# Performance work log

Hardware: AMD Instinct MI355X
Metric: run time of the kernel (lower is better)

## Reference

```python
import jax, jax.numpy as jnp
import numpy as np

IN_FEATURES = 4096
OUT_FEATURES = 4096
ALPHA = 0.008

def setup_inputs() -> dict:
    key = jax.random.key(0)
    k_x, k_w = jax.random.split(key)
    # int8-valued activations and weights, stored as their natural int/float forms
    x = jax.random.randint(k_x, (4, 2048, IN_FEATURES), -127, 128, dtype=jnp.int32)
    weight = jax.random.randint(k_w, (OUT_FEATURES, IN_FEATURES), -127, 128, dtype=jnp.int32).astype(jnp.float32)
    bias = jnp.zeros((1, OUT_FEATURES), dtype=jnp.float32)  # fp16 in module; fp32 here for math
    alpha = jnp.float32(ALPHA)
    return {"x": x, "weight": weight, "bias": bias, "alpha": alpha}

def reference(x, weight, bias, alpha):
    # x: [B, S, in], weight: [out, in] (int8 values cast to fp32), bias: [1, out]
    # In the original, rand_elements/mask_mul are zeros so hybrid path == plain path:
    #   y = F.linear(x.float(), weight.float()); fp_y = y*alpha + bias
    x_shape = x.shape
    xf = x.reshape(-1, x_shape[-1]).astype(jnp.float32)  # [N, in]
    y = jnp.einsum('ni,oi->no', xf, weight)              # fp32 GEMM, as in the module
    fp_y = y * alpha + bias
    out = jnp.clip(jnp.round(fp_y), -128, 127).astype(jnp.int8)
    return out.reshape(*x_shape[:-1], -1)
```

## Files before the change

kernel.cpp:

```cpp
#include <hip/hip_runtime.h>
#include <stdint.h>

typedef int int32x4  __attribute__((ext_vector_type(4)));
typedef int int32x16 __attribute__((ext_vector_type(16)));

#define IN_F   4096
#define OUT_F  4096
#define ROWS   8192

#define BM 256
#define BN 256
#define BK 64
#define NT (IN_F / BK)
#define ABUF 16384
#define LDS_TOTAL (4 * ABUF)

#define GLOAD_LDS16(g, l)                                                      \
  __builtin_amdgcn_global_load_lds(                                            \
      (const __attribute__((address_space(1))) void*)(g),                      \
      (__attribute__((address_space(3))) void*)(l), 16, 0, 0)

__device__ __forceinline__ int pack4i(int a, int b, int c, int d) {
  return (a & 0xff) | ((b & 0xff) << 8) | ((c & 0xff) << 16) | (d << 24);
}

#define CVT_BLOCKS 2048
#define CVT_NA 1048576
#define CVT_NTOT 1572864
__global__ void __launch_bounds__(256) cvt_kernel(const int4* __restrict__ x,
                                                  const float4* __restrict__ w,
                                                  int4* __restrict__ oa,
                                                  int4* __restrict__ ob) {
  for (size_t c = (size_t)blockIdx.x * 256 + threadIdx.x; c < CVT_NTOT;
       c += (size_t)CVT_BLOCKS * 256) {
    if (c < CVT_NA) {
      const int block = (int)(c >> 5), r = (int)(c & 31);
      const int m = (block >> 7) * 32 + r, kb = block & 127;
      const int4* src = x + (size_t)m * 1024 + kb * 8;
      int p[8];
#pragma unroll
      for (int j = 0; j < 8; ++j) {
        int4 a = src[j];
        p[j] = pack4i(a.x, a.y, a.z, a.w);
      }
      oa[(size_t)block * 64 + r]      = make_int4(p[0], p[1], p[2], p[3]);
      oa[(size_t)block * 64 + r + 32] = make_int4(p[4], p[5], p[6], p[7]);
    } else {
      const size_t c2 = c - CVT_NA;
      const int block = (int)(c2 >> 5), r = (int)(c2 & 31);
      const int n = (block >> 7) * 32 + r, kb = block & 127;
      const float4* src = w + (size_t)n * 1024 + kb * 8;
      int p[8];
#pragma unroll
      for (int j = 0; j < 8; ++j) {
        float4 a = src[j];
        p[j] = pack4i(__float2int_rn(a.x), __float2int_rn(a.y),
                      __float2int_rn(a.z), __float2int_rn(a.w));
      }
      ob[(size_t)block * 64 + r]      = make_int4(p[0], p[1], p[2], p[3]);
      ob[(size_t)block * 64 + r + 32] = make_int4(p[4], p[5], p[6], p[7]);
    }
  }
}

__global__ void __launch_bounds__(512) gemm_i8_kernel(
    const int8_t* __restrict__ A8p, const int8_t* __restrict__ B8p,
    const float* __restrict__ bias, const float* __restrict__ alpha_p,
    int* __restrict__ out) {
  extern __shared__ int8_t lds[];

  const int t    = threadIdx.x;
  const int wave = t >> 6;
  const int lane = t & 63;
  const int l31  = lane & 31;
  const int hi   = lane >> 5;
  const int wm   = wave >> 2;
  const int wn   = wave & 3;

  const int flat = blockIdx.y * gridDim.x + blockIdx.x;
  const int wid  = (flat & 7) * 64 + (flat >> 3);
  const int bn   = wid >> 5;
  const int bm   = wid & 31;

  const int mb0 = bm * 8 + (t >> 7);
  const int kbi = (t >> 6) & 1;
  const size_t aOff0 = ((size_t)mb0 * 128 + kbi) * 1024 + (size_t)(t & 63) * 16;
  const size_t aOff1 = ((size_t)(mb0 + 4) * 128 + kbi) * 1024 + (size_t)(t & 63) * 16;
  const int ldsT = t * 16;

  const int8_t* bPtr = B8p + (size_t)(bn * 8 + wn * 2) * 131072 + (size_t)lane * 16;

  const int aLds = wm * 8192 + lane * 16;

  int32x16 acc[4][2] = {};
  int32x4 af[4][2];
  int32x4 Bc00, Bc01, Bc10, Bc11, Bn00, Bn01, Bn10, Bn11;

#define ISSUE_A(TILE)                                                          \
  do {                                                                         \
    int8_t* _b = lds + ((TILE) & 3) * ABUF;                                    \
    GLOAD_LDS16(A8p + aOff0 + (size_t)(TILE) * 2048, _b + ldsT);               \
    GLOAD_LDS16(A8p + aOff1 + (size_t)(TILE) * 2048, _b + 8192 + ldsT);        \
  } while (0)

#define LOAD_B(TILE, B00, B01, B10, B11)                                       \
  do {                                                                         \
    const int8_t* _p = bPtr + (size_t)(TILE) * 2048;                           \
    B00 = *(const int32x4*)(_p);                                               \
    B01 = *(const int32x4*)(_p + 1024);                                        \
    B10 = *(const int32x4*)(_p + 131072);                                      \
    B11 = *(const int32x4*)(_p + 131072 + 1024);                               \
  } while (0)

#define READ_A(TILE)                                                           \
  do {                                                                         \
    const int8_t* _a = lds + ((TILE) & 3) * ABUF + aLds;                       \
    _Pragma("unroll") for (int mi = 0; mi < 4; ++mi) {                         \
      af[mi][0] = *(const int32x4*)(_a + mi * 2048);                           \
      af[mi][1] = *(const int32x4*)(_a + mi * 2048 + 1024);                    \
    }                                                                          \
  } while (0)

#define MFMA16(B00, B01, B10, B11)                                             \
  do {                                                                         \
    __builtin_amdgcn_s_setprio(1);                                             \
    _Pragma("unroll") for (int mi = 0; mi < 4; ++mi) {                         \
      acc[mi][0] = __builtin_amdgcn_mfma_i32_32x32x32_i8(af[mi][0], B00,       \
                                                         acc[mi][0], 0, 0, 0); \
      acc[mi][1] = __builtin_amdgcn_mfma_i32_32x32x32_i8(af[mi][0], B10,       \
                                                         acc[mi][1], 0, 0, 0); \
    }                                                                          \
    _Pragma("unroll") for (int mi = 0; mi < 4; ++mi) {                         \
      acc[mi][0] = __builtin_amdgcn_mfma_i32_32x32x32_i8(af[mi][1], B01,       \
                                                         acc[mi][0], 0, 0, 0); \
      acc[mi][1] = __builtin_amdgcn_mfma_i32_32x32x32_i8(af[mi][1], B11,       \
                                                         acc[mi][1], 0, 0, 0); \
    }                                                                          \
    __builtin_amdgcn_s_setprio(0);                                             \
  } while (0)

#define GATE2                                                                  \
  do {                                                                         \
    asm volatile("s_waitcnt vmcnt(2)" ::: "memory");                           \
    __builtin_amdgcn_s_barrier();                                              \
  } while (0)

  ISSUE_A(0);
  LOAD_B(0, Bc00, Bc01, Bc10, Bc11);
  ISSUE_A(1);
  GATE2;

  for (int tt = 0; tt < NT - 2; tt += 2) {
    LOAD_B(tt + 1, Bn00, Bn01, Bn10, Bn11);
    ISSUE_A(tt + 2);
    READ_A(tt);
    MFMA16(Bc00, Bc01, Bc10, Bc11);
    GATE2;

    LOAD_B(tt + 2, Bc00, Bc01, Bc10, Bc11);
    ISSUE_A(tt + 3);
    READ_A(tt + 1);
    MFMA16(Bn00, Bn01, Bn10, Bn11);
    GATE2;
  }
  LOAD_B(NT - 1, Bn00, Bn01, Bn10, Bn11);
  READ_A(NT - 2);
  MFMA16(Bc00, Bc01, Bc10, Bc11);
  asm volatile("s_waitcnt vmcnt(0)" ::: "memory");
  __builtin_amdgcn_s_barrier();
  READ_A(NT - 1);
  MFMA16(Bn00, Bn01, Bn10, Bn11);

  const float alpha = *alpha_p;
#pragma unroll
  for (int mi = 0; mi < 4; ++mi) {
    const int rowt = bm * BM + wm * 128 + mi * 32 + hi * 4;
#pragma unroll
    for (int ni = 0; ni < 2; ++ni) {
      const int col = bn * BN + wn * 64 + ni * 32 + l31;
      const float bv = bias[col];
#pragma unroll
      for (int r = 0; r < 16; ++r) {
        const int row = rowt + (r & 3) + 8 * (r >> 2);
        float v = rintf((float)acc[mi][ni][r] * alpha + bv);
        v = fminf(fmaxf(v, -128.f), 127.f);
        out[(size_t)row * OUT_F + col] = (int)v;
      }
    }
  }
#undef ISSUE_A
#undef LOAD_B
#undef READ_A
#undef MFMA16
#undef GATE2
}

extern "C" void kernel_launch(void* const* d_in, const int* in_sizes, int n_in,
                              void* d_out, int out_size, void* d_ws, size_t ws_size,
                              hipStream_t stream) {
  const int*   x     = (const int*)d_in[0];
  const float* w     = (const float*)d_in[1];
  const float* bias  = (const float*)d_in[2];
  const float* alpha = (const float*)d_in[3];
  int* out = (int*)d_out;

  int8_t* x8 = (int8_t*)d_ws;
  int8_t* w8 = x8 + (size_t)ROWS * IN_F;

  static bool attr_done = false;
  if (!attr_done) {
    (void)hipFuncSetAttribute(reinterpret_cast<const void*>(gemm_i8_kernel),
                              hipFuncAttributeMaxDynamicSharedMemorySize,
                              LDS_TOTAL);
    attr_done = true;
  }

  cvt_kernel<<<CVT_BLOCKS, 256, 0, stream>>>((const int4*)x, (const float4*)w,
                                             (int4*)x8, (int4*)w8);

  dim3 grid(OUT_F / BN, ROWS / BM);
  gemm_i8_kernel<<<grid, 512, LDS_TOTAL, stream>>>(x8, w8, bias, alpha, out);
}
```

Baseline: 417.0 us.

## Shrink GEMM tiles to 128x128 with 4 waves and remap convert kernel threads

The GEMM block tile goes from 256x256 with 8 waves to 128x128 with 4 waves, and each wave now holds a 64x64 output sub-tile. The LDS buffers shrink to match, and launch bounds ask for 3 blocks per CU. The aim is more blocks and better occupancy and load balance across CUs, at the cost of less data reuse per block and more global traffic for A and B. The convert kernel also changes its thread-to-element mapping so that each group of 8 adjacent threads handles 8 different k-blocks, which changes how its memory accesses coalesce.

```diff
diff --git a/kernel.cpp b/kernel.cpp
--- a/kernel.cpp
+++ b/kernel.cpp
@@ -8,11 +8,11 @@
 #define OUT_F  4096
 #define ROWS   8192
 
-#define BM 256
-#define BN 256
+#define BM 128
+#define BN 128
 #define BK 64
 #define NT (IN_F / BK)
-#define ABUF 16384
+#define ABUF 8192
 #define LDS_TOTAL (4 * ABUF)
 
 #define GLOAD_LDS16(g, l)                                                      \
@@ -31,10 +31,12 @@
                                                   const float4* __restrict__ w,
                                                   int4* __restrict__ oa,
                                                   int4* __restrict__ ob) {
-  for (size_t c = (size_t)blockIdx.x * 256 + threadIdx.x; c < CVT_NTOT;
-       c += (size_t)CVT_BLOCKS * 256) {
-    if (c < CVT_NA) {
-      const int block = (int)(c >> 5), r = (int)(c & 31);
+  const int t = threadIdx.x;
+  for (size_t base = (size_t)blockIdx.x * 256; base < CVT_NTOT;
+       base += (size_t)CVT_BLOCKS * 256) {
+    if (base < CVT_NA) {
+      const int block = (int)(base >> 5) + (t & 7);
+      const int r = t >> 3;
       const int m = (block >> 7) * 32 + r, kb = block & 127;
       const int4* src = x + (size_t)m * 1024 + kb * 8;
       int p[8];
@@ -46,8 +48,9 @@
       oa[(size_t)block * 64 + r]      = make_int4(p[0], p[1], p[2], p[3]);
       oa[(size_t)block * 64 + r + 32] = make_int4(p[4], p[5], p[6], p[7]);
     } else {
-      const size_t c2 = c - CVT_NA;
-      const int block = (int)(c2 >> 5), r = (int)(c2 & 31);
+      const size_t b2 = base - CVT_NA;
+      const int block = (int)(b2 >> 5) + (t & 7);
+      const int r = t >> 3;
       const int n = (block >> 7) * 32 + r, kb = block & 127;
       const float4* src = w + (size_t)n * 1024 + kb * 8;
       int p[8];
@@ -63,7 +66,7 @@
   }
 }
 
-__global__ void __launch_bounds__(512) gemm_i8_kernel(
+__global__ void __launch_bounds__(256, 3) gemm_i8_kernel(
     const int8_t* __restrict__ A8p, const int8_t* __restrict__ B8p,
     const float* __restrict__ bias, const float* __restrict__ alpha_p,
     int* __restrict__ out) {
@@ -74,33 +77,32 @@
   const int lane = t & 63;
   const int l31  = lane & 31;
   const int hi   = lane >> 5;
-  const int wm   = wave >> 2;
-  const int wn   = wave & 3;
+  const int wm   = wave >> 1;
+  const int wn   = wave & 1;
 
   const int flat = blockIdx.y * gridDim.x + blockIdx.x;
-  const int wid  = (flat & 7) * 64 + (flat >> 3);
-  const int bn   = wid >> 5;
-  const int bm   = wid & 31;
-
-  const int mb0 = bm * 8 + (t >> 7);
-  const int kbi = (t >> 6) & 1;
-  const size_t aOff0 = ((size_t)mb0 * 128 + kbi) * 1024 + (size_t)(t & 63) * 16;
-  const size_t aOff1 = ((size_t)(mb0 + 4) * 128 + kbi) * 1024 + (size_t)(t & 63) * 16;
+  const int wid  = (flat & 7) * 256 + (flat >> 3);
+  const int bn   = wid >> 6;
+  const int bm   = wid & 63;
+
+  const int ebT = t >> 7, kbT = (t >> 6) & 1, lT = t & 63;
+  const size_t aOff0 = ((size_t)(bm * 4 + ebT) * 128 + kbT) * 1024 + lT * 16;
+  const size_t aOff1 = ((size_t)(bm * 4 + ebT + 2) * 128 + kbT) * 1024 + lT * 16;
   const int ldsT = t * 16;
 
-  const int8_t* bPtr = B8p + (size_t)(bn * 8 + wn * 2) * 131072 + (size_t)lane * 16;
-
-  const int aLds = wm * 8192 + lane * 16;
-
-  int32x16 acc[4][2] = {};
-  int32x4 af[4][2];
+  const int8_t* bPtr = B8p + (size_t)(bn * 4 + wn * 2) * 131072 + (size_t)lane * 16;
+
+  const int aLds = wm * 4096 + lane * 16;
+
+  int32x16 acc[2][2] = {};
+  int32x4 af[2][2];
   int32x4 Bc00, Bc01, Bc10, Bc11, Bn00, Bn01, Bn10, Bn11;
 
 #define ISSUE_A(TILE)                                                          \
   do {                                                                         \
     int8_t* _b = lds + ((TILE) & 3) * ABUF;                                    \
     GLOAD_LDS16(A8p + aOff0 + (size_t)(TILE) * 2048, _b + ldsT);               \
-    GLOAD_LDS16(A8p + aOff1 + (size_t)(TILE) * 2048, _b + 8192 + ldsT);        \
+    GLOAD_LDS16(A8p + aOff1 + (size_t)(TILE) * 2048, _b + 4096 + ldsT);        \
   } while (0)
 
 #define LOAD_B(TILE, B00, B01, B10, B11)                                       \
@@ -115,27 +117,31 @@
 #define READ_A(TILE)                                                           \
   do {                                                                         \
     const int8_t* _a = lds + ((TILE) & 3) * ABUF + aLds;                       \
-    _Pragma("unroll") for (int mi = 0; mi < 4; ++mi) {                         \
+    _Pragma("unroll") for (int mi = 0; mi < 2; ++mi) {                         \
       af[mi][0] = *(const int32x4*)(_a + mi * 2048);                           \
       af[mi][1] = *(const int32x4*)(_a + mi * 2048 + 1024);                    \
     }                                                                          \
   } while (0)
 
-#define MFMA16(B00, B01, B10, B11)                                             \
+#define MFMA8(B00, B01, B10, B11)                                              \
   do {                                                                         \
     __builtin_amdgcn_s_setprio(1);                                             \
-    _Pragma("unroll") for (int mi = 0; mi < 4; ++mi) {                         \
-      acc[mi][0] = __builtin_amdgcn_mfma_i32_32x32x32_i8(af[mi][0], B00,       \
-                                                         acc[mi][0], 0, 0, 0); \
-      acc[mi][1] = __builtin_amdgcn_mfma_i32_32x32x32_i8(af[mi][0], B10,       \
-                                                         acc[mi][1], 0, 0, 0); \
-    }                                                                          \
-    _Pragma("unroll") for (int mi = 0; mi < 4; ++mi) {                         \
-      acc[mi][0] = __builtin_amdgcn_mfma_i32_32x32x32_i8(af[mi][1], B01,       \
-                                                         acc[mi][0], 0, 0, 0); \
-      acc[mi][1] = __builtin_amdgcn_mfma_i32_32x32x32_i8(af[mi][1], B11,       \
-                                                         acc[mi][1], 0, 0, 0); \
-    }                                                                          \
+    acc[0][0] = __builtin_amdgcn_mfma_i32_32x32x32_i8(af[0][0], B00,           \
+                                                      acc[0][0], 0, 0, 0);     \
+    acc[0][1] = __builtin_amdgcn_mfma_i32_32x32x32_i8(af[0][0], B10,           \
+                                                      acc[0][1], 0, 0, 0);     \
+    acc[1][0] = __builtin_amdgcn_mfma_i32_32x32x32_i8(af[1][0], B00,           \
+                                                      acc[1][0], 0, 0, 0);     \
+    acc[1][1] = __builtin_amdgcn_mfma_i32_32x32x32_i8(af[1][0], B10,           \
+                                                      acc[1][1], 0, 0, 0);     \
+    acc[0][0] = __builtin_amdgcn_mfma_i32_32x32x32_i8(af[0][1], B01,           \
+                                                      acc[0][0], 0, 0, 0);     \
+    acc[0][1] = __builtin_amdgcn_mfma_i32_32x32x32_i8(af[0][1], B11,           \
+                                                      acc[0][1], 0, 0, 0);     \
+    acc[1][0] = __builtin_amdgcn_mfma_i32_32x32x32_i8(af[1][1], B01,           \
+                                                      acc[1][0], 0, 0, 0);     \
+    acc[1][1] = __builtin_amdgcn_mfma_i32_32x32x32_i8(af[1][1], B11,           \
+                                                      acc[1][1], 0, 0, 0);     \
     __builtin_amdgcn_s_setprio(0);                                             \
   } while (0)
 
@@ -154,27 +160,27 @@
     LOAD_B(tt + 1, Bn00, Bn01, Bn10, Bn11);
     ISSUE_A(tt + 2);
     READ_A(tt);
-    MFMA16(Bc00, Bc01, Bc10, Bc11);
+    MFMA8(Bc00, Bc01, Bc10, Bc11);
     GATE2;
 
     LOAD_B(tt + 2, Bc00, Bc01, Bc10, Bc11);
     ISSUE_A(tt + 3);
     READ_A(tt + 1);
-    MFMA16(Bn00, Bn01, Bn10, Bn11);
+    MFMA8(Bn00, Bn01, Bn10, Bn11);
     GATE2;
   }
   LOAD_B(NT - 1, Bn00, Bn01, Bn10, Bn11);
   READ_A(NT - 2);
-  MFMA16(Bc00, Bc01, Bc10, Bc11);
+  MFMA8(Bc00, Bc01, Bc10, Bc11);
   asm volatile("s_waitcnt vmcnt(0)" ::: "memory");
   __builtin_amdgcn_s_barrier();
   READ_A(NT - 1);
-  MFMA16(Bn00, Bn01, Bn10, Bn11);
+  MFMA8(Bn00, Bn01, Bn10, Bn11);
 
   const float alpha = *alpha_p;
 #pragma unroll
-  for (int mi = 0; mi < 4; ++mi) {
-    const int rowt = bm * BM + wm * 128 + mi * 32 + hi * 4;
+  for (int mi = 0; mi < 2; ++mi) {
+    const int rowt = bm * BM + wm * 64 + mi * 32 + hi * 4;
 #pragma unroll
     for (int ni = 0; ni < 2; ++ni) {
       const int col = bn * BN + wn * 64 + ni * 32 + l31;
@@ -191,7 +197,7 @@
 #undef ISSUE_A
 #undef LOAD_B
 #undef READ_A
-#undef MFMA16
+#undef MFMA8
 #undef GATE2
 }
 
@@ -219,5 +225,5 @@
                                              (int4*)x8, (int4*)w8);
 
   dim3 grid(OUT_F / BN, ROWS / BM);
-  gemm_i8_kernel<<<grid, 512, LDS_TOTAL, stream>>>(x8, w8, bias, alpha, out);
-}
+  gemm_i8_kernel<<<grid, 256, LDS_TOTAL, stream>>>(x8, w8, bias, alpha, out);
+}
```

Result: slower. 437.4 us (+4.9%).
